# Optimization experiments

Measured on AMD Instinct MI355X. Metric: run time of the kernel, lower is better.

The kernel has to match this reference:

```python
import jax, jax.numpy as jnp
import numpy as np

N_NODES = 32768
N_EDGES = 196608
N_GRAPHS = 256
DEG = 6
HID = 128
RVD = 16
EMB = HID - RVD   # atom/bond embedding dim = hidden - random_vec_dim
VOCAB = 128
TGT = 256
DEPTH = 5
N_AGG = 4         # mean, max, min, std
N_SC = 3          # identity, amplification, attenuation
EPS = 1e-5


def setup_inputs() -> dict:
    key = jax.random.key(0)
    ks = jax.random.split(key, 12)

    def g(i, shape, scale=0.05):
        return jax.random.normal(ks[i], shape, dtype=jnp.float32) * scale

    return {
        "atom_feats": jax.random.randint(ks[0], (N_NODES, 9), 0, 100),
        "bond_feats": jax.random.randint(ks[1], (N_EDGES, 3), 0, 4),
        "src": jax.random.randint(ks[2], (N_EDGES,), 0, N_NODES),
        # every node receives exactly DEG messages (DGL reduce requires in-edges)
        "dst": jnp.repeat(jnp.arange(N_NODES), DEG),
        "graph_ids": jnp.repeat(jnp.arange(N_GRAPHS), N_NODES // N_GRAPHS),
        "n_graphs": N_GRAPHS,
        "rand_x": jax.random.normal(ks[3], (N_NODES, RVD), dtype=jnp.float32),   # std=1.0
        "rand_edge": jax.random.normal(ks[4], (N_EDGES, RVD), dtype=jnp.float32),
        "atom_emb": g(5, (9, VOCAB, EMB)),
        "bond_emb": g(6, (3, VOCAB, EMB)),
        "pre_W": g(7, (DEPTH, 3 * HID, HID)),
        "pre_b": jnp.zeros((DEPTH, HID), jnp.float32),
        "post_W": g(8, (DEPTH, (N_AGG * N_SC + 1) * HID, HID)),
        "post_b": jnp.zeros((DEPTH, HID), jnp.float32),
        "ro_W1": g(9, (3 * HID, HID)),
        "ro_b1": jnp.zeros((HID,), jnp.float32),
        "ro_W2": g(10, (HID, TGT)),
        "ro_b2": jnp.zeros((TGT,), jnp.float32),
    }


def reference(atom_feats, bond_feats, src, dst, graph_ids, n_graphs,
              rand_x, rand_edge, atom_emb, bond_emb,
              pre_W, pre_b, post_W, post_b, ro_W1, ro_b1, ro_W2, ro_b2):
    n = atom_feats.shape[0]
    # OGB-style encoders: sum of per-column embeddings, then concat random vec
    h = jnp.concatenate([atom_emb[jnp.arange(9), atom_feats].sum(1), rand_x], -1)   # [N, HID]
    ef = jnp.concatenate([bond_emb[jnp.arange(3), bond_feats].sum(1), rand_edge], -1)  # [E, HID]

    deg = jax.ops.segment_sum(jnp.ones((dst.shape[0],), h.dtype), dst, n)
    degc = jnp.maximum(deg, 1.0)[:, None]
    logD = jnp.log(deg + 1.0)[:, None]                 # avg_d['log'] = 1.0
    inv_logD = jnp.where(logD > 0, 1.0 / jnp.maximum(logD, EPS), 0.0)

    def layer(hc, p):
        pW, pb, qW, qb = p
        # pretrans MLP on [src_feat, dst_feat, edge_feat]; last_activation = activation (relu)
        z = jnp.concatenate([hc[src], hc[dst], ef], -1)          # [E, 3*HID]
        e = jax.nn.relu(z @ pW + pb)                             # [E, HID]
        s = jax.ops.segment_sum(e, dst, n)
        mean = s / degc
        mean_sq = jax.ops.segment_sum(e * e, dst, n) / degc
        mx = jax.ops.segment_max(e, dst, n)
        mn = jax.ops.segment_min(e, dst, n)
        std = jnp.sqrt(jax.nn.relu(mean_sq - mean * mean) + EPS)
        agg = jnp.concatenate([mean, mx, mn, std], -1)           # [N, 4*HID]
        scaled = jnp.concatenate([agg, agg * logD, agg * inv_logD], -1)  # [N, 12*HID]
        h_new = jnp.concatenate([hc, scaled], -1) @ qW + qb + hc  # posttrans (linear) + residual
        return h_new, None

    h, _ = jax.lax.scan(layer, h, (pre_W, pre_b, post_W, post_b))

    # multi-aggregator readout: mean, sum, max per graph
    cnt = jnp.maximum(jax.ops.segment_sum(jnp.ones((n,), h.dtype), graph_ids, n_graphs), 1.0)[:, None]
    gsum = jax.ops.segment_sum(h, graph_ids, n_graphs)
    gmax = jax.ops.segment_max(h, graph_ids, n_graphs)
    r = jnp.concatenate([gsum / cnt, gsum, gmax], -1)            # [G, 3*HID]
    return jax.nn.relu(r @ ro_W1 + ro_b1) @ ro_W2 + ro_b2        # [G, TGT]
```

## Files before the change

kernel.cpp:

```cpp
#include <hip/hip_runtime.h>
#include <hip/hip_bf16.h>

#define N_NODES 32768
#define N_EDGES 196608
#define N_GRAPHS 256
#define DEG 6
#define HID 128
#define RVD 16
#define EMB 112
#define VOCAB 128
#define TGT 256
#define DEPTH 5

#define LOG7 1.9459101090932196f
#define ILOG7 0.5138983423697507f

typedef __hip_bfloat16 bf16;
using frag_ab = __attribute__((ext_vector_type(8))) short;
using frag_cd = __attribute__((ext_vector_type(4))) float;

static __device__ __forceinline__ float b2f(bf16 x) { return __bfloat162float(x); }
static __device__ __forceinline__ bf16  f2b(float x) { return __float2bfloat16(x); }
static __device__ __forceinline__ short f2s(float x) {
    bf16 b = __float2bfloat16(x);
    return *reinterpret_cast<short*>(&b);
}
static __device__ __forceinline__ float us2f(unsigned short u) {
    unsigned int x = ((unsigned int)u) << 16;
    return __uint_as_float(x);
}
static __device__ __forceinline__ unsigned short f2us(float x) {
    bf16 b = __float2bfloat16(x);
    return *reinterpret_cast<unsigned short*>(&b);
}

#define PB_ENC  16384
#define PB_WB   (PB_ENC + 640)
#define PB_WC   (PB_WB + 1600)
#define PB_WR   (PB_WC + 80)
#define PB_CODE (PB_WR + 768)
#define PB_T    (PB_CODE + 320)

__global__ __launch_bounds__(256) void prep_k(const int* __restrict__ af, const float* __restrict__ rx,
                                              const float* __restrict__ aemb, bf16* __restrict__ h,
                                              const float* __restrict__ preW, const float* __restrict__ preB,
                                              const float* __restrict__ postW,
                                              const int* __restrict__ bfeat, const float* __restrict__ bemb,
                                              bf16* __restrict__ wb, bf16* __restrict__ wc,
                                              bf16* __restrict__ wrB, unsigned char* __restrict__ codeA,
                                              bf16* __restrict__ Tb) {
    int blk = blockIdx.x, tid = threadIdx.x;
    if (blk < PB_ENC) {
        int v = blk * 2 + (tid >> 7), c = tid & 127;
        float val;
        if (c < EMB) {
            val = 0.f;
            #pragma unroll
            for (int i = 0; i < 9; ++i) {
                int f = af[v * 9 + i];
                val += aemb[(i * VOCAB + f) * EMB + c];
            }
        } else {
            val = rx[v * RVD + (c - EMB)];
        }
        h[(size_t)v * HID + c] = f2b(val);
    } else if (blk < PB_WB) {
        int idx = (blk - PB_ENC) * 256 + tid;
        if (idx < DEPTH * 32768) {
            int j = idx & 7, L = (idx >> 3) & 63, nt = (idx >> 9) & 15, ks = (idx >> 13) & 3, l = idx >> 15;
            int k = ks * 32 + ((L >> 4) * 8) + j;
            int n = nt * 16 + (L & 15);
            const float* W = preW + (size_t)l * 384 * 128;
            float v = (n < 128) ? W[k * 128 + n] : W[(128 + k) * 128 + (n - 128)];
            wb[idx] = f2b(v);
        }
    } else if (blk < PB_WC) {
        int idx = (blk - PB_WB) * 256 + tid;
        if (idx < DEPTH * 81920) {
            int j = idx & 7, L = (idx >> 3) & 63, nt = (idx >> 9) & 7;
            int t = idx >> 12;
            int ks = t % 20, l = t / 20;
            int k = ks * 32 + ((L >> 4) * 8) + j;
            int n = nt * 16 + (L & 15);
            const float* W = postW + (size_t)l * 1664 * 128;
            float v;
            if (k < 128) {
                v = W[k * 128 + n];
            } else {
                int jj = k - 128;
                v = W[(128 + jj) * 128 + n] + LOG7 * W[(640 + jj) * 128 + n] + ILOG7 * W[(1152 + jj) * 128 + n];
            }
            wc[idx] = f2b(v);
        }
    } else if (blk < PB_WR) {
        int idx = (blk - PB_WC) * 256 + tid;
        if (idx < DEPTH * 4096) {
            int j = idx & 7, L = (idx >> 3) & 63, nt = (idx >> 9) & 7, l = idx >> 12;
            int k = ((L >> 4) * 8) + j;
            int n = nt * 16 + (L & 15);
            float v = (k < 16) ? preW[(size_t)l * 384 * 128 + (368 + k) * 128 + n] : 0.f;
            wrB[idx] = f2b(v);
        }
    } else if (blk < PB_CODE) {
        int e = (blk - PB_WR) * 256 + tid;
        if (e < N_EDGES)
            codeA[e] = (unsigned char)(bfeat[e * 3] | (bfeat[e * 3 + 1] << 2) | (bfeat[e * 3 + 2] << 4));
    } else {
        if (tid < 128) {
            int t = blk - PB_CODE;
            int l = t >> 6, cd = t & 63, c = tid;
            int f0 = cd & 3, f1 = (cd >> 2) & 3, f2 = cd >> 4;
            const float* W = preW + (size_t)l * 384 * 128 + 256 * 128;
            float acc = preB[l * 128 + c];
            #pragma unroll 4
            for (int k = 0; k < EMB; ++k) {
                float bsk = bemb[(0 * VOCAB + f0) * EMB + k]
                          + bemb[(1 * VOCAB + f1) * EMB + k]
                          + bemb[(2 * VOCAB + f2) * EMB + k];
                acc += bsk * W[k * 128 + c];
            }
            Tb[(size_t)(l * 64 + cd) * 128 + c] = f2b(acc);
        }
    }
}

__global__ __launch_bounds__(256) void gemm_z12(const bf16* __restrict__ A,
                                                const bf16* __restrict__ Bp,
                                                bf16* __restrict__ C) {
    int lane = threadIdx.x & 63;
    int wave = threadIdx.x >> 6;
    int m = lane & 15, quad = lane >> 4;
    int row0 = blockIdx.x * 64 + wave * 16;

    frag_cd acc[16];
    #pragma unroll
    for (int nt = 0; nt < 16; ++nt)
        #pragma unroll
        for (int i = 0; i < 4; ++i) acc[nt][i] = 0.f;

    const frag_ab* Bf = (const frag_ab*)Bp;
    const bf16* arow = A + (size_t)(row0 + m) * 128;
    #pragma unroll
    for (int ks = 0; ks < 4; ++ks) {
        frag_ab a = *(const frag_ab*)(arow + ks * 32 + quad * 8);
        #pragma unroll
        for (int nt = 0; nt < 16; ++nt) {
            frag_ab b = Bf[(ks * 16 + nt) * 64 + lane];
            acc[nt] = __builtin_amdgcn_mfma_f32_16x16x32_bf16(a, b, acc[nt], 0, 0, 0);
        }
    }
    #pragma unroll
    for (int nt = 0; nt < 16; ++nt) {
        int col = nt * 16 + m;
        #pragma unroll
        for (int r = 0; r < 4; ++r) {
            int row = row0 + quad * 4 + r;
            C[(size_t)row * 256 + col] = f2b(acc[nt][r]);
        }
    }
}

__global__ __launch_bounds__(512, 4) void fused_layer(bf16* __restrict__ h,
                                                      const bf16* __restrict__ Zcur,
                                                      const int* __restrict__ src,
                                                      const unsigned char* __restrict__ code,
                                                      const float* __restrict__ rand_edge,
                                                      const bf16* __restrict__ Tb,
                                                      const bf16* __restrict__ WrB,
                                                      const bf16* __restrict__ Bp,
                                                      const float* __restrict__ bias,
                                                      const bf16* __restrict__ Bn,
                                                      bf16* __restrict__ Znext) {
    __shared__ __align__(16) bf16 agg_lds[64 * 520];
    __shared__ __align__(16) bf16 rdot[48 * 136];

    int tid = threadIdx.x;
    int lane = tid & 63, wave = tid >> 6;
    int m = lane & 15, quad = lane >> 4;
    int row0 = blockIdx.x * 64;

    const unsigned short* Zu = (const unsigned short*)Zcur;
    const unsigned short* Tu = (const unsigned short*)Tb;
    const unsigned short* Ru = (const unsigned short*)rdot;
    unsigned short* Ag = (unsigned short*)agg_lds;
    int c = lane * 2;

    for (int r = 0; r < 8; ++r) {
        int bv = row0 + r * 8;
        if (wave < 3) {
            frag_ab a;
            if (quad < 2) {
                const float4* rp = (const float4*)(rand_edge
                    + (size_t)(bv * 6 + wave * 16 + m) * 16 + quad * 8);
                float4 A = rp[0], B = rp[1];
                a[0] = f2s(A.x); a[1] = f2s(A.y); a[2] = f2s(A.z); a[3] = f2s(A.w);
                a[4] = f2s(B.x); a[5] = f2s(B.y); a[6] = f2s(B.z); a[7] = f2s(B.w);
            } else {
                #pragma unroll
                for (int j = 0; j < 8; ++j) a[j] = 0;
            }
            const frag_ab* Bf = (const frag_ab*)WrB;
            #pragma unroll
            for (int nt = 0; nt < 8; ++nt) {
                frag_cd acc;
                #pragma unroll
                for (int i = 0; i < 4; ++i) acc[i] = 0.f;
                acc = __builtin_amdgcn_mfma_f32_16x16x32_bf16(a, Bf[nt * 64 + lane], acc, 0, 0, 0);
                #pragma unroll
                for (int rr = 0; rr < 4; ++rr)
                    rdot[(wave * 16 + quad * 4 + rr) * 136 + nt * 16 + m] = f2b(acc[rr]);
            }
        }
        __syncthreads();
        {
            int nb = wave;
            int v = bv + nb;
            ushort2 z2u = *(const ushort2*)(Zu + (size_t)v * 256 + 128 + c);
            float z2a = us2f(z2u.x), z2b = us2f(z2u.y);
            const int2* sp = (const int2*)(src + v * 6);
            int2 s01 = sp[0], s23 = sp[1], s45 = sp[2];
            const unsigned short* cp = (const unsigned short*)(code + v * 6);
            unsigned short c01 = cp[0], c23 = cp[1], c45 = cp[2];
            int svs[6] = { s01.x, s01.y, s23.x, s23.y, s45.x, s45.y };
            int cds[6] = { c01 & 255, c01 >> 8, c23 & 255, c23 >> 8, c45 & 255, c45 >> 8 };
            ushort2 z1u[6], tvu[6];
            #pragma unroll
            for (int j = 0; j < 6; ++j) z1u[j] = *(const ushort2*)(Zu + (size_t)svs[j] * 256 + c);
            #pragma unroll
            for (int j = 0; j < 6; ++j) tvu[j] = *(const ushort2*)(Tu + cds[j] * 128 + c);
            float sa = 0.f, ssa = 0.f, mxa = -1e30f, mna = 1e30f;
            float sb = 0.f, ssb = 0.f, mxb = -1e30f, mnb = 1e30f;
            #pragma unroll
            for (int j = 0; j < 6; ++j) {
                ushort2 rdu = *(const ushort2*)(Ru + (nb * 6 + j) * 136 + c);
                float va = us2f(z1u[j].x) + z2a + us2f(tvu[j].x) + us2f(rdu.x);
                float vb = us2f(z1u[j].y) + z2b + us2f(tvu[j].y) + us2f(rdu.y);
                va = fmaxf(va, 0.f);
                vb = fmaxf(vb, 0.f);
                sa += va; ssa += va * va; mxa = fmaxf(mxa, va); mna = fminf(mna, va);
                sb += vb; ssb += vb * vb; mxb = fmaxf(mxb, vb); mnb = fminf(mnb, vb);
            }
            float meana = sa * (1.f / 6.f), meanb = sb * (1.f / 6.f);
            float msqa = ssa * (1.f / 6.f), msqb = ssb * (1.f / 6.f);
            float sda = sqrtf(fmaxf(msqa - meana * meana, 0.f) + 1e-5f);
            float sdb = sqrtf(fmaxf(msqb - meanb * meanb, 0.f) + 1e-5f);
            int lrow = r * 8 + nb;
            size_t base = (size_t)lrow * 520 + c;
            *(ushort2*)(Ag + base)       = make_ushort2(f2us(meana), f2us(meanb));
            *(ushort2*)(Ag + base + 128) = make_ushort2(f2us(mxa),  f2us(mxb));
            *(ushort2*)(Ag + base + 256) = make_ushort2(f2us(mna),  f2us(mnb));
            *(ushort2*)(Ag + base + 384) = make_ushort2(f2us(sda),  f2us(sdb));
        }
        __syncthreads();
    }

    int rt = wave & 3, nh = wave >> 2;
    int rowA = row0 + rt * 16 + m;

    frag_cd acc[4];
    #pragma unroll
    for (int nt = 0; nt < 4; ++nt)
        #pragma unroll
        for (int i = 0; i < 4; ++i) acc[nt][i] = 0.f;

    const frag_ab* Bf = (const frag_ab*)Bp;
    const bf16* arow = h + (size_t)rowA * 128;
    #pragma unroll
    for (int ks = 0; ks < 4; ++ks) {
        frag_ab a = *(const frag_ab*)(arow + ks * 32 + quad * 8);
        #pragma unroll
        for (int nt = 0; nt < 4; ++nt) {
            frag_ab b = Bf[(ks * 8 + nh * 4 + nt) * 64 + lane];
            acc[nt] = __builtin_amdgcn_mfma_f32_16x16x32_bf16(a, b, acc[nt], 0, 0, 0);
        }
    }
    const bf16* grow = agg_lds + (size_t)(rt * 16 + m) * 520;
    #pragma unroll
    for (int ks = 0; ks < 16; ++ks) {
        frag_ab a = *(const frag_ab*)(grow + ks * 32 + quad * 8);
        #pragma unroll
        for (int nt = 0; nt < 4; ++nt) {
            frag_ab b = Bf[((4 + ks) * 8 + nh * 4 + nt) * 64 + lane];
            acc[nt] = __builtin_amdgcn_mfma_f32_16x16x32_bf16(a, b, acc[nt], 0, 0, 0);
        }
    }

    __syncthreads();

    bf16* newh = agg_lds;
    #pragma unroll
    for (int nt = 0; nt < 4; ++nt) {
        int col = nh * 64 + nt * 16 + m;
        float bs_ = bias[col];
        #pragma unroll
        for (int r2 = 0; r2 < 4; ++r2) {
            int lr = rt * 16 + quad * 4 + r2;
            int row = row0 + lr;
            float nv = acc[nt][r2] + bs_ + b2f(h[(size_t)row * HID + col]);
            bf16 bv2 = f2b(nv);
            h[(size_t)row * HID + col] = bv2;
            newh[lr * 136 + col] = bv2;
        }
    }

    if (Bn) {
        __syncthreads();
        const frag_ab* Bf2 = (const frag_ab*)Bn;
        frag_cd a2[8];
        #pragma unroll
        for (int nt = 0; nt < 8; ++nt)
            #pragma unroll
            for (int i = 0; i < 4; ++i) a2[nt][i] = 0.f;
        #pragma unroll
        for (int ks = 0; ks < 4; ++ks) {
            frag_ab a = *(const frag_ab*)&newh[(rt * 16 + m) * 136 + ks * 32 + quad * 8];
            #pragma unroll
            for (int nt = 0; nt < 8; ++nt) {
                frag_ab b = Bf2[(ks * 16 + nh * 8 + nt) * 64 + lane];
                a2[nt] = __builtin_amdgcn_mfma_f32_16x16x32_bf16(a, b, a2[nt], 0, 0, 0);
            }
        }
        #pragma unroll
        for (int nt = 0; nt < 8; ++nt) {
            int col = nh * 128 + nt * 16 + m;
            #pragma unroll
            for (int r2 = 0; r2 < 4; ++r2) {
                int row = row0 + rt * 16 + quad * 4 + r2;
                Znext[(size_t)row * 256 + col] = f2b(a2[nt][r2]);
            }
        }
    }
}

__global__ __launch_bounds__(128) void readout(const bf16* __restrict__ h, const float* __restrict__ W1,
                                               const float* __restrict__ b1, const float* __restrict__ W2,
                                               const float* __restrict__ b2, float* __restrict__ out) {
    __shared__ float r[384];
    __shared__ float y1[128];
    int g = blockIdx.x, c = threadIdx.x;
    float s = 0.f, mx = -1e30f;
    for (int v = 0; v < 128; ++v) {
        float hv = b2f(h[((size_t)g * 128 + v) * HID + c]);
        s += hv; mx = fmaxf(mx, hv);
    }
    r[c] = s * (1.f / 128.f);
    r[128 + c] = s;
    r[256 + c] = mx;
    __syncthreads();
    float a1 = b1[c];
    for (int k = 0; k < 384; ++k) a1 += r[k] * W1[k * 128 + c];
    y1[c] = fmaxf(a1, 0.f);
    __syncthreads();
    #pragma unroll
    for (int o = 0; o < 2; ++o) {
        int t = c + o * 128;
        float a2 = b2[t];
        for (int k = 0; k < 128; ++k) a2 += y1[k] * W2[k * 256 + t];
        out[(size_t)g * 256 + t] = a2;
    }
}

extern "C" void kernel_launch(void* const* d_in, const int* in_sizes, int n_in,
                              void* d_out, int out_size, void* d_ws, size_t ws_size,
                              hipStream_t stream) {
    const int*   atom_feats = (const int*)d_in[0];
    const int*   bond_feats = (const int*)d_in[1];
    const int*   src        = (const int*)d_in[2];
    const float* rand_x     = (const float*)d_in[6];
    const float* rand_edge  = (const float*)d_in[7];
    const float* atom_emb   = (const float*)d_in[8];
    const float* bond_emb   = (const float*)d_in[9];
    const float* pre_W      = (const float*)d_in[10];
    const float* pre_b      = (const float*)d_in[11];
    const float* post_W     = (const float*)d_in[12];
    const float* post_b     = (const float*)d_in[13];
    const float* ro_W1      = (const float*)d_in[14];
    const float* ro_b1      = (const float*)d_in[15];
    const float* ro_W2      = (const float*)d_in[16];
    const float* ro_b2      = (const float*)d_in[17];

    char* p = (char*)d_ws;
    auto alloc = [&](size_t bytes) {
        char* r = p;
        p += (bytes + 255) & ~(size_t)255;
        return r;
    };
    bf16*  h    = (bf16*) alloc((size_t)N_NODES * HID * 2);
    bf16*  z12a = (bf16*) alloc((size_t)N_NODES * 256 * 2);
    bf16*  z12b = (bf16*) alloc((size_t)N_NODES * 256 * 2);
    bf16*  wb   = (bf16*) alloc((size_t)DEPTH * 32768 * 2);
    bf16*  wc   = (bf16*) alloc((size_t)DEPTH * 81920 * 2);
    bf16*  wrB  = (bf16*) alloc((size_t)DEPTH * 4096 * 2);
    bf16*  Tb   = (bf16*) alloc((size_t)DEPTH * 64 * 128 * 2);
    unsigned char* code = (unsigned char*)alloc(N_EDGES);

    prep_k<<<PB_T, 256, 0, stream>>>(atom_feats, rand_x, atom_emb, h,
                                     pre_W, pre_b, post_W,
                                     bond_feats, bond_emb,
                                     wb, wc, wrB, code, Tb);

    gemm_z12<<<N_NODES / 64, 256, 0, stream>>>(h, wb, z12a);

    bf16* zc = z12a;
    bf16* zn = z12b;
    for (int l = 0; l < DEPTH; ++l) {
        const bf16* wbn = (l + 1 < DEPTH) ? (wb + (size_t)(l + 1) * 32768) : nullptr;
        fused_layer<<<N_NODES / 64, 512, 0, stream>>>(
            h, zc, src, code, rand_edge,
            Tb + (size_t)l * 8192,
            wrB + (size_t)l * 4096,
            wc + (size_t)l * 81920,
            post_b + l * HID,
            wbn, zn);
        bf16* t = zc; zc = zn; zn = t;
    }

    readout<<<N_GRAPHS, 128, 0, stream>>>(h, ro_W1, ro_b1, ro_W2, ro_b2, (float*)d_out);
}
```

Before: 344.3 us.

## Compute rand-edge projection with per-lane FMAs and software-pipeline neighbor gathers per wave

The per-edge random-vector projection (16x128) is now computed directly in fp32 by each lane with register-held weight columns, replacing the MFMA pass that wrote results to shared memory. Each wave now processes 8 consecutive nodes independently, double-buffering src/code indices and neighbor Z/T gathers one node ahead, and staging rand_edge rows through a per-wave LDS buffer. This removes the per-row block-wide __syncthreads pairs and idle waves during the MFMA step, and is meant to hide gather latency. In exchange it adds 16 FMAs per element on vector ALUs, raises register pressure, and changes the precision of that term from bf16 to fp32.

```diff
diff --git a/kernel.cpp b/kernel.cpp
--- a/kernel.cpp
+++ b/kernel.cpp
@@ -18,13 +18,10 @@
 typedef __hip_bfloat16 bf16;
 using frag_ab = __attribute__((ext_vector_type(8))) short;
 using frag_cd = __attribute__((ext_vector_type(4))) float;
+typedef float f32x2 __attribute__((ext_vector_type(2)));
 
 static __device__ __forceinline__ float b2f(bf16 x) { return __bfloat162float(x); }
 static __device__ __forceinline__ bf16  f2b(float x) { return __float2bfloat16(x); }
-static __device__ __forceinline__ short f2s(float x) {
-    bf16 b = __float2bfloat16(x);
-    return *reinterpret_cast<short*>(&b);
-}
 static __device__ __forceinline__ float us2f(unsigned short u) {
     unsigned int x = ((unsigned int)u) << 16;
     return __uint_as_float(x);
@@ -166,13 +163,13 @@
                                                       const unsigned char* __restrict__ code,
                                                       const float* __restrict__ rand_edge,
                                                       const bf16* __restrict__ Tb,
-                                                      const bf16* __restrict__ WrB,
+                                                      const float* __restrict__ Wr,
                                                       const bf16* __restrict__ Bp,
                                                       const float* __restrict__ bias,
                                                       const bf16* __restrict__ Bn,
                                                       bf16* __restrict__ Znext) {
     __shared__ __align__(16) bf16 agg_lds[64 * 520];
-    __shared__ __align__(16) bf16 rdot[48 * 136];
+    __shared__ __align__(16) float relds[8][384];
 
     int tid = threadIdx.x;
     int lane = tid & 63, wave = tid >> 6;
@@ -181,78 +178,118 @@
 
     const unsigned short* Zu = (const unsigned short*)Zcur;
     const unsigned short* Tu = (const unsigned short*)Tb;
-    const unsigned short* Ru = (const unsigned short*)rdot;
     unsigned short* Ag = (unsigned short*)agg_lds;
     int c = lane * 2;
 
-    for (int r = 0; r < 8; ++r) {
-        int bv = row0 + r * 8;
-        if (wave < 3) {
-            frag_ab a;
-            if (quad < 2) {
-                const float4* rp = (const float4*)(rand_edge
-                    + (size_t)(bv * 6 + wave * 16 + m) * 16 + quad * 8);
-                float4 A = rp[0], B = rp[1];
-                a[0] = f2s(A.x); a[1] = f2s(A.y); a[2] = f2s(A.z); a[3] = f2s(A.w);
-                a[4] = f2s(B.x); a[5] = f2s(B.y); a[6] = f2s(B.z); a[7] = f2s(B.w);
-            } else {
+    {
+        const int vbase = row0 + wave * 8;
+
+        f32x2 wr2[16];
+        #pragma unroll
+        for (int k = 0; k < 16; ++k) {
+            float2 w2 = *(const float2*)(Wr + k * 128 + c);
+            wr2[k].x = w2.x; wr2[k].y = w2.y;
+        }
+
+        {
+            const float2* rb = (const float2*)(rand_edge + (size_t)vbase * 96);
+            float2 a0 = rb[lane], a1 = rb[lane + 64], a2 = rb[lane + 128];
+            float2* rl = (float2*)relds[wave];
+            rl[lane] = a0; rl[lane + 64] = a1; rl[lane + 128] = a2;
+        }
+        float2 rh0, rh1, rh2;
+
+        int svs[2][6]; int cds[2][6];
+        ushort2 z1u[2][6], tvu[2][6], z2u[2];
+
+        {
+            const int2* sp = (const int2*)(src + vbase * 6);
+            int2 a = sp[0], b = sp[1], d = sp[2];
+            svs[0][0] = a.x; svs[0][1] = a.y; svs[0][2] = b.x;
+            svs[0][3] = b.y; svs[0][4] = d.x; svs[0][5] = d.y;
+            const unsigned short* cp = (const unsigned short*)(code + vbase * 6);
+            unsigned short x = cp[0], y = cp[1], z = cp[2];
+            cds[0][0] = x & 255; cds[0][1] = x >> 8; cds[0][2] = y & 255;
+            cds[0][3] = y >> 8;  cds[0][4] = z & 255; cds[0][5] = z >> 8;
+        }
+        z2u[0] = *(const ushort2*)(Zu + (size_t)vbase * 256 + 128 + c);
+        #pragma unroll
+        for (int j = 0; j < 6; ++j) z1u[0][j] = *(const ushort2*)(Zu + (size_t)svs[0][j] * 256 + c);
+        #pragma unroll
+        for (int j = 0; j < 6; ++j) tvu[0][j] = *(const ushort2*)(Tu + cds[0][j] * 128 + c);
+        {
+            const int2* sp = (const int2*)(src + (vbase + 1) * 6);
+            int2 a = sp[0], b = sp[1], d = sp[2];
+            svs[1][0] = a.x; svs[1][1] = a.y; svs[1][2] = b.x;
+            svs[1][3] = b.y; svs[1][4] = d.x; svs[1][5] = d.y;
+            const unsigned short* cp = (const unsigned short*)(code + (vbase + 1) * 6);
+            unsigned short x = cp[0], y = cp[1], z = cp[2];
+            cds[1][0] = x & 255; cds[1][1] = x >> 8; cds[1][2] = y & 255;
+            cds[1][3] = y >> 8;  cds[1][4] = z & 255; cds[1][5] = z >> 8;
+        }
+
+        #pragma unroll
+        for (int i = 0; i < 8; ++i) {
+            const int s = i & 1, t = s ^ 1;
+            if (i == 2) {
+                const float2* rb2 = (const float2*)(rand_edge + (size_t)(vbase + 4) * 96);
+                rh0 = rb2[lane]; rh1 = rb2[lane + 64]; rh2 = rb2[lane + 128];
+            }
+            if (i == 4) {
+                float2* rl = (float2*)relds[wave];
+                rl[lane] = rh0; rl[lane + 64] = rh1; rl[lane + 128] = rh2;
+            }
+            if (i < 7) {
+                z2u[t] = *(const ushort2*)(Zu + (size_t)(vbase + i + 1) * 256 + 128 + c);
                 #pragma unroll
-                for (int j = 0; j < 8; ++j) a[j] = 0;
-            }
-            const frag_ab* Bf = (const frag_ab*)WrB;
-            #pragma unroll
-            for (int nt = 0; nt < 8; ++nt) {
-                frag_cd acc;
+                for (int j = 0; j < 6; ++j) z1u[t][j] = *(const ushort2*)(Zu + (size_t)svs[t][j] * 256 + c);
                 #pragma unroll
-                for (int i = 0; i < 4; ++i) acc[i] = 0.f;
-                acc = __builtin_amdgcn_mfma_f32_16x16x32_bf16(a, Bf[nt * 64 + lane], acc, 0, 0, 0);
-                #pragma unroll
-                for (int rr = 0; rr < 4; ++rr)
-                    rdot[(wave * 16 + quad * 4 + rr) * 136 + nt * 16 + m] = f2b(acc[rr]);
-            }
-        }
-        __syncthreads();
-        {
-            int nb = wave;
-            int v = bv + nb;
-            ushort2 z2u = *(const ushort2*)(Zu + (size_t)v * 256 + 128 + c);
-            float z2a = us2f(z2u.x), z2b = us2f(z2u.y);
-            const int2* sp = (const int2*)(src + v * 6);
-            int2 s01 = sp[0], s23 = sp[1], s45 = sp[2];
-            const unsigned short* cp = (const unsigned short*)(code + v * 6);
-            unsigned short c01 = cp[0], c23 = cp[1], c45 = cp[2];
-            int svs[6] = { s01.x, s01.y, s23.x, s23.y, s45.x, s45.y };
-            int cds[6] = { c01 & 255, c01 >> 8, c23 & 255, c23 >> 8, c45 & 255, c45 >> 8 };
-            ushort2 z1u[6], tvu[6];
-            #pragma unroll
-            for (int j = 0; j < 6; ++j) z1u[j] = *(const ushort2*)(Zu + (size_t)svs[j] * 256 + c);
-            #pragma unroll
-            for (int j = 0; j < 6; ++j) tvu[j] = *(const ushort2*)(Tu + cds[j] * 128 + c);
-            float sa = 0.f, ssa = 0.f, mxa = -1e30f, mna = 1e30f;
-            float sb = 0.f, ssb = 0.f, mxb = -1e30f, mnb = 1e30f;
+                for (int j = 0; j < 6; ++j) tvu[t][j] = *(const ushort2*)(Tu + cds[t][j] * 128 + c);
+            }
+            if (i < 6) {
+                const int2* sp = (const int2*)(src + (vbase + i + 2) * 6);
+                int2 a = sp[0], b = sp[1], d = sp[2];
+                svs[s][0] = a.x; svs[s][1] = a.y; svs[s][2] = b.x;
+                svs[s][3] = b.y; svs[s][4] = d.x; svs[s][5] = d.y;
+                const unsigned short* cp = (const unsigned short*)(code + (vbase + i + 2) * 6);
+                unsigned short x = cp[0], y = cp[1], z = cp[2];
+                cds[s][0] = x & 255; cds[s][1] = x >> 8; cds[s][2] = y & 255;
+                cds[s][3] = y >> 8;  cds[s][4] = z & 255; cds[s][5] = z >> 8;
+            }
+
+            float z2a = us2f(z2u[s].x), z2b = us2f(z2u[s].y);
+            f32x2 s2  = {0.f, 0.f}, ss2 = {0.f, 0.f};
+            f32x2 mx2 = {-1e30f, -1e30f}, mn2 = {1e30f, 1e30f};
             #pragma unroll
             for (int j = 0; j < 6; ++j) {
-                ushort2 rdu = *(const ushort2*)(Ru + (nb * 6 + j) * 136 + c);
-                float va = us2f(z1u[j].x) + z2a + us2f(tvu[j].x) + us2f(rdu.x);
-                float vb = us2f(z1u[j].y) + z2b + us2f(tvu[j].y) + us2f(rdu.y);
-                va = fmaxf(va, 0.f);
-                vb = fmaxf(vb, 0.f);
-                sa += va; ssa += va * va; mxa = fmaxf(mxa, va); mna = fminf(mna, va);
-                sb += vb; ssb += vb * vb; mxb = fmaxf(mxb, vb); mnb = fminf(mnb, vb);
-            }
-            float meana = sa * (1.f / 6.f), meanb = sb * (1.f / 6.f);
-            float msqa = ssa * (1.f / 6.f), msqb = ssb * (1.f / 6.f);
-            float sda = sqrtf(fmaxf(msqa - meana * meana, 0.f) + 1e-5f);
-            float sdb = sqrtf(fmaxf(msqb - meanb * meanb, 0.f) + 1e-5f);
-            int lrow = r * 8 + nb;
+                const float4* rp = (const float4*)&relds[wave][(i & 3) * 96 + j * 16];
+                float4 r0 = rp[0], r1 = rp[1], r2 = rp[2], r3 = rp[3];
+                f32x2 v2;
+                v2.x = us2f(z1u[s][j].x) + z2a + us2f(tvu[s][j].x);
+                v2.y = us2f(z1u[s][j].y) + z2b + us2f(tvu[s][j].y);
+                float rk[16] = {r0.x, r0.y, r0.z, r0.w, r1.x, r1.y, r1.z, r1.w,
+                                r2.x, r2.y, r2.z, r2.w, r3.x, r3.y, r3.z, r3.w};
+                #pragma unroll
+                for (int k = 0; k < 16; ++k) v2 += rk[k] * wr2[k];
+                v2 = __builtin_elementwise_max(v2, (f32x2){0.f, 0.f});
+                s2 += v2;
+                ss2 += v2 * v2;
+                mx2 = __builtin_elementwise_max(mx2, v2);
+                mn2 = __builtin_elementwise_min(mn2, v2);
+            }
+            f32x2 mean2 = s2 * (1.f / 6.f);
+            f32x2 msq2  = ss2 * (1.f / 6.f);
+            f32x2 var2  = __builtin_elementwise_max(msq2 - mean2 * mean2, (f32x2){0.f, 0.f});
+            float sda = sqrtf(var2.x + 1e-5f), sdb = sqrtf(var2.y + 1e-5f);
+            int lrow = wave * 8 + i;
             size_t base = (size_t)lrow * 520 + c;
-            *(ushort2*)(Ag + base)       = make_ushort2(f2us(meana), f2us(meanb));
-            *(ushort2*)(Ag + base + 128) = make_ushort2(f2us(mxa),  f2us(mxb));
-            *(ushort2*)(Ag + base + 256) = make_ushort2(f2us(mna),  f2us(mnb));
-            *(ushort2*)(Ag + base + 384) = make_ushort2(f2us(sda),  f2us(sdb));
-        }
-        __syncthreads();
-    }
+            *(ushort2*)(Ag + base)       = make_ushort2(f2us(mean2.x), f2us(mean2.y));
+            *(ushort2*)(Ag + base + 128) = make_ushort2(f2us(mx2.x),   f2us(mx2.y));
+            *(ushort2*)(Ag + base + 256) = make_ushort2(f2us(mn2.x),   f2us(mn2.y));
+            *(ushort2*)(Ag + base + 384) = make_ushort2(f2us(sda),     f2us(sdb));
+        }
+    }
+    __syncthreads();
 
     int rt = wave & 3, nh = wave >> 2;
     int rowA = row0 + rt * 16 + m;
@@ -408,7 +445,7 @@
         fused_layer<<<N_NODES / 64, 512, 0, stream>>>(
             h, zc, src, code, rand_edge,
             Tb + (size_t)l * 8192,
-            wrB + (size_t)l * 4096,
+            pre_W + (size_t)l * 384 * 128 + 368 * 128,
             wc + (size_t)l * 81920,
             post_b + l * HID,
             wbn, zn);
```

Result: no change. 337.7 us (-1.9%).
